# Kernel optimization log

Measured on AMD Instinct MI355X. Metric: run time of the kernel, lower is better.

## Reference

```python
import jax, jax.numpy as jnp
import numpy as np
from jax import lax

B0, C0, H0, W0 = 4, 128, 48, 48
GR = 32  # growth rate
NL = 4   # dense layers


def conv1x1(x, w, b):
    # w: [O, Cin], x: [B, Cin, H, W]
    return jnp.einsum('oc,bchw->bohw', w, x) + b[None, :, None, None]


def conv3x3(x, w, b):
    y = lax.conv_general_dilated(x, w, (1, 1), [(1, 1), (1, 1)],
                                 dimension_numbers=('NCHW', 'OIHW', 'NCHW'))
    return y + b[None, :, None, None]


def batchnorm(x, g, b, eps=1e-5):
    # training-mode BatchNorm2d: batch statistics over (B, H, W)
    mu = jnp.mean(x, axis=(0, 2, 3), keepdims=True)
    var = jnp.var(x, axis=(0, 2, 3), keepdims=True)
    return (x - mu) * lax.rsqrt(var + eps) * g[None, :, None, None] + b[None, :, None, None]


def apply_rope(x):
    B, C, H, W = x.shape
    half = C // 2
    theta = 1.0 / (10000.0 ** (jnp.arange(half, dtype=x.dtype) / half))
    # pos_emb[h, w, j] = (h + w) * theta[j]
    pos = (jnp.arange(H, dtype=x.dtype)[:, None, None]
           + jnp.arange(W, dtype=x.dtype)[None, :, None]) * theta
    cos = jnp.cos(pos).transpose(2, 0, 1)  # [half, H, W]
    sin = jnp.sin(pos).transpose(2, 0, 1)
    xr = x.reshape(B, half, 2, H, W)
    x_re, x_im = xr[:, :, 0], xr[:, :, 1]
    rr = x_re * cos - x_im * sin
    ri = x_re * sin + x_im * cos
    return jnp.stack([rr, ri], axis=2).reshape(B, C, H, W)


def setup_inputs() -> dict:
    key = jax.random.key(0)
    ks = iter(jax.random.split(key, 64))
    def nrm(shape, s=0.05):
        return jax.random.normal(next(ks), shape, jnp.float32) * s
    C = C0
    dc = C + NL * GR  # 256 dense-block output channels
    hid = 4 * C
    d = {
        'x': jax.random.normal(next(ks), (B0, C0, H0, W0), jnp.float32),
        'r_w': nrm((C, C)), 'r_b': jnp.zeros((C,), jnp.float32),
        'k_w': nrm((C, C)), 'k_b': jnp.zeros((C,), jnp.float32),
        'v_w': nrm((C, C)), 'v_b': jnp.zeros((C,), jnp.float32),
        'wc1_w': nrm((C // 4, C, 3, 3)), 'wc1_b': jnp.zeros((C // 4,), jnp.float32),
        'wc2_w': nrm((C, C // 4)), 'wc2_b': jnp.zeros((C,), jnp.float32),
        'u': nrm((C,), 0.1),
        'sn1_w': nrm((dc // 4, dc)), 'sn1_b': jnp.zeros((dc // 4,), jnp.float32),
        'sn2_w': nrm((dc, dc // 4)), 'sn2_b': jnp.zeros((dc,), jnp.float32),
        'lb_w': nrm((C // 4, dc)), 'lb_b': jnp.zeros((C // 4,), jnp.float32),
        'ld_w': nrm((C // 4, dc)), 'ld_b': jnp.zeros((C // 4,), jnp.float32),
        'ps_w': nrm((C, C // 4)), 'ps_b': jnp.zeros((C,), jnp.float32),
        'pq_w': nrm((C, C)), 'pq_b': jnp.zeros((C,), jnp.float32),
        'fc1_w': nrm((hid, C)), 'fc1_b': jnp.zeros((hid,), jnp.float32),
        'fc2_w': nrm((C, hid)), 'fc2_b': jnp.zeros((C,), jnp.float32),
    }
    for i in range(NL):
        cin = C + i * GR
        d[f'db_g{i}'] = jnp.ones((cin,), jnp.float32)
        d[f'db_b{i}'] = jnp.zeros((cin,), jnp.float32)
        d[f'db_w{i}'] = nrm((GR, cin, 3, 3))
        d[f'db_cb{i}'] = jnp.zeros((GR,), jnp.float32)
    return d


def _forward(x, r_w, r_b, k_w, k_b, v_w, v_b, wc1_w, wc1_b, wc2_w, wc2_b, u,
             db_g0, db_b0, db_w0, db_cb0, db_g1, db_b1, db_w1, db_cb1,
             db_g2, db_b2, db_w2, db_cb2, db_g3, db_b3, db_w3, db_cb3,
             sn1_w, sn1_b, sn2_w, sn2_b, lb_w, lb_b, ld_w, ld_b,
             ps_w, ps_b, pq_w, pq_b, fc1_w, fc1_b, fc2_w, fc2_b):
    B, C, H, W = x.shape
    N = H * W
    # decay gate w (hidden is None so it multiplies zeros, kept for fidelity)
    w_gate = jax.nn.sigmoid(conv1x1(jax.nn.relu(conv3x3(x, wc1_w, wc1_b)), wc2_w, wc2_b)).reshape(B, C, N)
    x_rope = apply_rope(x)
    r = jax.nn.sigmoid(conv1x1(x, r_w, r_b))
    k = conv1x1(x_rope, k_w, k_b).reshape(B, C, N)
    v = conv1x1(x_rope, v_w, v_b).reshape(B, C, N)
    zeros = jnp.zeros_like(k)
    new_num = zeros * jnp.exp(-w_gate) + k * v
    new_den = zeros * jnp.exp(-w_gate) + k
    eu = jnp.exp(u)[None, :, None]
    wkv = ((new_num + eu * k * v) / (new_den + eu * k)).reshape(B, C, H, W)
    recursive_output = r * wkv
    # dense block (concat-growth)
    feats = x
    for g, bb, wt, cb in ((db_g0, db_b0, db_w0, db_cb0), (db_g1, db_b1, db_w1, db_cb1),
                          (db_g2, db_b2, db_w2, db_cb2), (db_g3, db_b3, db_w3, db_cb3)):
        h = jax.nn.relu(batchnorm(feats, g, bb))
        feats = jnp.concatenate([feats, conv3x3(h, wt, cb)], axis=1)
    df = feats  # [B, C+4*GR, H, W]
    # adaptive spiking neuron
    tau = jnp.mean(jax.nn.sigmoid(conv1x1(jax.nn.relu(conv1x1(df, sn1_w, sn1_b)), sn2_w, sn2_b)),
                   axis=(2, 3), keepdims=True)
    spike_prob = jax.nn.sigmoid((df - 1.0) * 5.0)
    sf = spike_prob * (df * jnp.exp(-1.0 / (tau + 1e-6))) + (1.0 - spike_prob) * df
    # first attention over N tokens, channels = C//4
    Bf = conv1x1(sf, lb_w, lb_b).reshape(B, -1, N)
    Df = conv1x1(sf, ld_w, ld_b).reshape(B, -1, N)
    attn = jax.nn.softmax(jnp.einsum('bcn,bcm->bnm', Bf, Bf), axis=-1)
    att1 = jnp.einsum('bnm,bcm->bcn', attn, Df).reshape(B, -1, H, W)
    spike_output = conv1x1(att1, ps_w, ps_b)
    combined = recursive_output + spike_output
    # second attention (k/v convs are shared with WKV path)
    Q = conv1x1(combined, pq_w, pq_b).reshape(B, C, N)
    K = conv1x1(combined, k_w, k_b).reshape(B, C, N)
    V = conv1x1(combined, v_w, v_b).reshape(B, C, N)
    scores = jnp.einsum('bcn,bcm->bnm', Q, K) / jnp.sqrt(jnp.asarray(C, x.dtype))
    aw = jax.nn.softmax(scores, axis=-1)
    att2 = jnp.einsum('bnm,bcm->bcn', aw, V).reshape(B, C, H, W)
    x1 = x + att2
    out = x1 + conv1x1(jax.nn.relu(conv1x1(x1, fc1_w, fc1_b)) ** 2, fc2_w, fc2_b)
    return out, new_num, new_den


def reference(x, r_w, r_b, k_w, k_b, v_w, v_b, wc1_w, wc1_b, wc2_w, wc2_b, u,
              db_g0, db_b0, db_w0, db_cb0, db_g1, db_b1, db_w1, db_cb1,
              db_g2, db_b2, db_w2, db_cb2, db_g3, db_b3, db_w3, db_cb3,
              sn1_w, sn1_b, sn2_w, sn2_b, lb_w, lb_b, ld_w, ld_b,
              ps_w, ps_b, pq_w, pq_b, fc1_w, fc1_b, fc2_w, fc2_b):
    return _forward(x, r_w, r_b, k_w, k_b, v_w, v_b, wc1_w, wc1_b, wc2_w, wc2_b, u,
                    db_g0, db_b0, db_w0, db_cb0, db_g1, db_b1, db_w1, db_cb1,
                    db_g2, db_b2, db_w2, db_cb2, db_g3, db_b3, db_w3, db_cb3,
                    sn1_w, sn1_b, sn2_w, sn2_b, lb_w, lb_b, ld_w, ld_b,
                    ps_w, ps_b, pq_w, pq_b, fc1_w, fc1_b, fc2_w, fc2_b)
```

## Files before the change

### kernel.cpp

```cpp
#include <hip/hip_runtime.h>
#include <math.h>

#define BB 4
#define CC 128
#define HH 48
#define WW 48
#define NSP (HH*WW)
#define DCC 256
#define BCN (BB*CC*NSP)
#define KS 6

typedef float f32x4 __attribute__((ext_vector_type(4)));
typedef __bf16 bf16x8 __attribute__((ext_vector_type(8)));
typedef __bf16 bf16x4 __attribute__((ext_vector_type(4)));

__device__ __forceinline__ float sigmf(float v) { return 1.0f / (1.0f + __expf(-v)); }

struct Prep {
  const float* wsrc[13];
  int wlen[13];
  int woff[13];
  const float* psrc[4];
  int pcin[4];
  int poff[4];
  const float* x;
  float* sums;
  float* sums2;
  __bf16* x_t;
  __bf16* xrope_t;
};
__global__ __launch_bounds__(256) void prep_kernel(Prep a, __bf16* __restrict__ wdst,
                                                   __bf16* __restrict__ pdst) {
  __shared__ float lds[32][33];
  __shared__ float rs[4], rs2[4];
  int g = blockIdx.y;
  int idx = blockIdx.x * 256 + threadIdx.x;
  if (g < 13) {
    if (idx < a.wlen[g]) wdst[a.woff[g] + idx] = (__bf16)a.wsrc[g][idx];
  } else if (g < 17) {
    int L = g - 13;
    int cin = a.pcin[L];
    if (idx < 9 * 32 * cin) {
      int c = idx % cin;
      int o = (idx / cin) % 32;
      int tap = idx / (cin * 32);
      pdst[a.poff[L] + idx] = (__bf16)a.psrc[L][((size_t)o * cin + c) * 9 + tap];
    }
  } else if (g == 17) {
    int c = blockIdx.x;
    if (c >= 128) return;
    float s = 0.f, s2 = 0.f;
    for (int i = threadIdx.x; i < BB * NSP; i += 256) {
      int b = i / NSP, n = i % NSP;
      float v = a.x[((size_t)b * 128 + c) * NSP + n];
      s += v;
      s2 += v * v;
    }
#pragma unroll
    for (int off = 32; off > 0; off >>= 1) {
      s += __shfl_down(s, off);
      s2 += __shfl_down(s2, off);
    }
    int wid = threadIdx.x >> 6;
    if ((threadIdx.x & 63) == 0) { rs[wid] = s; rs2[wid] = s2; }
    __syncthreads();
    if (threadIdx.x == 0) {
      a.sums[c] = rs[0] + rs[1] + rs[2] + rs[3];
      a.sums2[c] = rs2[0] + rs2[1] + rs2[2] + rs2[3];
    }
  } else {
    int T = (g - 18) * 256 + blockIdx.x;
    if (T >= 1152) return;
    int b = T / 288;
    int r = T % 288;
    int c0 = (r / 72) * 32;
    int n0 = (r % 72) * 32;
    int tid = threadIdx.x;
    int nn = tid & 31, cs = tid >> 5;
#pragma unroll
    for (int j = 0; j < 4; ++j) {
      int cc = c0 + cs * 4 + j;
      lds[cs * 4 + j][nn] = a.x[((size_t)b * 128 + cc) * NSP + n0 + nn];
    }
    __syncthreads();
    int c = tid & 31, ns = tid >> 5;
#pragma unroll
    for (int j = 0; j < 4; ++j) {
      int n2 = ns * 4 + j;
      float pv = lds[c][n2];
      a.x_t[((size_t)b * NSP + n0 + n2) * 128 + c0 + c] = (__bf16)pv;
      int gc = c0 + c;
      int i = gc >> 1;
      float re = lds[c & ~1][n2];
      float im = lds[c | 1][n2];
      int n = n0 + n2;
      int h = n / WW, w = n % WW;
      float theta = __expf(-9.2103403719761836f * ((float)i) / 64.0f);
      float pos = (float)(h + w) * theta;
      float cs_ = cosf(pos), sn_ = sinf(pos);
      float vr_ = (gc & 1) ? (re * sn_ + im * cs_) : (re * cs_ - im * sn_);
      a.xrope_t[((size_t)b * NSP + n0 + n2) * 128 + c0 + c] = (__bf16)vr_;
    }
  }
}

__global__ __launch_bounds__(256) void kvr_kernel(
    const __bf16* __restrict__ xrope_t, const __bf16* __restrict__ x_t,
    const __bf16* __restrict__ wk, const __bf16* __restrict__ wvp,
    const __bf16* __restrict__ wr,
    const float* __restrict__ k_b, const float* __restrict__ v_b,
    const float* __restrict__ r_b, const float* __restrict__ u,
    float* __restrict__ kden, float* __restrict__ knum, float* __restrict__ rec) {
  int tid = threadIdx.x;
  int wv = tid >> 6, lane = tid & 63;
  int m15 = lane & 15, quad = lane >> 4;
  int b = blockIdx.y;
  int n0 = blockIdx.x * 16;
  int o0 = wv * 32;
  int n = n0 + m15;
  const __bf16* brr = xrope_t + ((size_t)b * NSP + n) * 128 + quad * 8;
  const __bf16* brx = x_t + ((size_t)b * NSP + n) * 128 + quad * 8;
  const __bf16* ak0 = wk + (size_t)(o0 + m15) * 128 + quad * 8;
  const __bf16* ak1 = wk + (size_t)(o0 + 16 + m15) * 128 + quad * 8;
  const __bf16* av0 = wvp + (size_t)(o0 + m15) * 128 + quad * 8;
  const __bf16* av1 = wvp + (size_t)(o0 + 16 + m15) * 128 + quad * 8;
  const __bf16* ar0 = wr + (size_t)(o0 + m15) * 128 + quad * 8;
  const __bf16* ar1 = wr + (size_t)(o0 + 16 + m15) * 128 + quad * 8;
  f32x4 fk[2], fv[2], fr[2];
#pragma unroll
  for (int t = 0; t < 2; ++t) {
    fk[t] = (f32x4){0.f, 0.f, 0.f, 0.f};
    fv[t] = (f32x4){0.f, 0.f, 0.f, 0.f};
    fr[t] = (f32x4){0.f, 0.f, 0.f, 0.f};
  }
#pragma unroll
  for (int kc = 0; kc < 128; kc += 32) {
    bf16x8 br_ = *(const bf16x8*)(brr + kc);
    bf16x8 bx_ = *(const bf16x8*)(brx + kc);
    fk[0] = __builtin_amdgcn_mfma_f32_16x16x32_bf16(*(const bf16x8*)(ak0 + kc), br_, fk[0], 0, 0, 0);
    fk[1] = __builtin_amdgcn_mfma_f32_16x16x32_bf16(*(const bf16x8*)(ak1 + kc), br_, fk[1], 0, 0, 0);
    fv[0] = __builtin_amdgcn_mfma_f32_16x16x32_bf16(*(const bf16x8*)(av0 + kc), br_, fv[0], 0, 0, 0);
    fv[1] = __builtin_amdgcn_mfma_f32_16x16x32_bf16(*(const bf16x8*)(av1 + kc), br_, fv[1], 0, 0, 0);
    fr[0] = __builtin_amdgcn_mfma_f32_16x16x32_bf16(*(const bf16x8*)(ar0 + kc), bx_, fr[0], 0, 0, 0);
    fr[1] = __builtin_amdgcn_mfma_f32_16x16x32_bf16(*(const bf16x8*)(ar1 + kc), bx_, fr[1], 0, 0, 0);
  }
#pragma unroll
  for (int t = 0; t < 2; ++t) {
#pragma unroll
    for (int reg = 0; reg < 4; ++reg) {
      int ol = o0 + t * 16 + quad * 4 + reg;
      float kk = fk[t][reg] + k_b[ol];
      float vv = fv[t][reg] + v_b[ol];
      float rr = sigmf(fr[t][reg] + r_b[ol]);
      float eu = __expf(u[ol]);
      size_t idx = ((size_t)b * 128 + ol) * NSP + n;
      float nv = kk * vv, tt = eu * kk;
      kden[idx] = kk;
      knum[idx] = nv;
      rec[idx] = rr * ((nv + tt * vv) / (kk + tt));
    }
  }
}

template <int OUT>
__device__ __forceinline__ void gemm_store(void* outp, int b, int n, int Oseg,
                                           int obase, int quad, const float* vr) {
  if (OUT == 0) {
    float* op = (float*)outp;
#pragma unroll
    for (int reg = 0; reg < 4; ++reg)
      op[((size_t)b * Oseg + obase + quad * 4 + reg) * NSP + n] = vr[reg];
  } else if (OUT == 1) {
    __bf16* op = (__bf16*)outp;
    bf16x4 pk;
#pragma unroll
    for (int reg = 0; reg < 4; ++reg) pk[reg] = (__bf16)vr[reg];
    *(bf16x4*)(op + ((size_t)b * NSP + n) * Oseg + obase + quad * 4) = pk;
  } else {
    __bf16* op = (__bf16*)outp;
#pragma unroll
    for (int reg = 0; reg < 4; ++reg)
      op[((size_t)b * Oseg + obase + quad * 4 + reg) * NSP + n] = (__bf16)vr[reg];
  }
}

template <int K, int ACT, int OUT0, int OUT1, int OUT2, int SPLITB>
__global__ __launch_bounds__(256) void gemm_mfma_kernel(
    const __bf16* __restrict__ in_t, const __bf16* __restrict__ in_t2,
    const __bf16* __restrict__ wb,
    const float* __restrict__ bias0, const float* __restrict__ bias1,
    const float* __restrict__ bias2,
    const float* __restrict__ add0, const float* __restrict__ add1,
    void* __restrict__ out0, void* __restrict__ out1, void* __restrict__ out2,
    int osplit, int osplit2, int Ototal, float sc0, float sc1, float sc2) {
  int tid = threadIdx.x;
  int wv = tid >> 6, lane = tid & 63;
  int m15 = lane & 15, quad = lane >> 4;
  int b = blockIdx.y;
  int n0 = blockIdx.x * 16;
  int wpb = blockDim.x >> 6;
  int o0 = (blockIdx.z * wpb + wv) * 32;
  if (o0 >= Ototal) return;
  int n = n0 + m15;
  const __bf16* brow = in_t + ((size_t)b * NSP + n) * (SPLITB ? 128 : K) + quad * 8;
  const __bf16* brow2 = SPLITB ? (in_t2 + ((size_t)b * NSP + n) * 128 + quad * 8) : nullptr;
  const __bf16* a0p = wb + (size_t)(o0 + m15) * K + quad * 8;
  const __bf16* a1p = wb + (size_t)(o0 + 16 + m15) * K + quad * 8;
  f32x4 of0 = (f32x4){0.f, 0.f, 0.f, 0.f};
  f32x4 of1 = (f32x4){0.f, 0.f, 0.f, 0.f};
#pragma unroll
  for (int kc = 0; kc < K; kc += 32) {
    bf16x8 bfr;
    if constexpr (SPLITB) {
      bfr = (kc < 128) ? *(const bf16x8*)(brow + kc) : *(const bf16x8*)(brow2 + (kc - 128));
    } else {
      bfr = *(const bf16x8*)(brow + kc);
    }
    bf16x8 a0 = *(const bf16x8*)(a0p + kc);
    bf16x8 a1 = *(const bf16x8*)(a1p + kc);
    of0 = __builtin_amdgcn_mfma_f32_16x16x32_bf16(a0, bfr, of0, 0, 0, 0);
    of1 = __builtin_amdgcn_mfma_f32_16x16x32_bf16(a1, bfr, of1, 0, 0, 0);
  }
  int seg = (o0 >= osplit2) ? 2 : (o0 >= osplit) ? 1 : 0;
  int segb = (seg == 2) ? osplit2 : (seg == 1) ? osplit : 0;
  int sege = (seg == 2) ? Ototal : (seg == 1) ? osplit2 : osplit;
  int Oseg = sege - segb;
  int ol0 = o0 - segb;
  const float* bias = (seg == 2) ? bias2 : (seg == 1) ? bias1 : bias0;
  const float* add = (seg == 2) ? nullptr : (seg == 1) ? add1 : add0;
  void* outp = (seg == 2) ? out2 : (seg == 1) ? out1 : out0;
  float sc = (seg == 2) ? sc2 : (seg == 1) ? sc1 : sc0;
#pragma unroll
  for (int t = 0; t < 2; ++t) {
    f32x4 acc = t ? of1 : of0;
    float vr[4];
#pragma unroll
    for (int reg = 0; reg < 4; ++reg) {
      int ol = ol0 + t * 16 + quad * 4 + reg;
      float v = acc[reg] + bias[ol];
      if (ACT == 1) v = fmaxf(v, 0.0f);
      else if (ACT == 2) v = sigmf(v);
      else if (ACT == 3) { v = fmaxf(v, 0.0f); v = v * v; }
      v *= sc;
      if (add) v += add[((size_t)b * Oseg + ol) * NSP + n];
      vr[reg] = v;
    }
    if constexpr (OUT0 == 3) {
#pragma unroll
      for (int reg = 0; reg < 4; ++reg) {
        float sv = vr[reg];
        sv += __shfl_xor(sv, 1);
        sv += __shfl_xor(sv, 2);
        sv += __shfl_xor(sv, 4);
        sv += __shfl_xor(sv, 8);
        if (m15 == 0)
          ((float*)out0)[((size_t)(b * DCC + ol0 + t * 16 + quad * 4 + reg)) * 144 +
                         blockIdx.x] = sv;
      }
    } else {
      if (seg == 0) gemm_store<OUT0>(outp, b, n, Oseg, ol0 + t * 16, quad, vr);
      else if (seg == 1) gemm_store<OUT1>(outp, b, n, Oseg, ol0 + t * 16, quad, vr);
      else gemm_store<OUT2>(outp, b, n, Oseg, ol0 + t * 16, quad, vr);
    }
  }
}

__global__ __launch_bounds__(128) void lbld_sf_kernel(
    const __bf16* __restrict__ x_t, const __bf16* __restrict__ dense_t,
    const float* __restrict__ taupart, const __bf16* __restrict__ wlb,
    const float* __restrict__ lb_b, const float* __restrict__ ld_b,
    __bf16* __restrict__ Bft, __bf16* __restrict__ Dfb) {
  __shared__ float ef[256];
  int tid = threadIdx.x;
  int b = blockIdx.y;
  for (int ch = tid; ch < 256; ch += 128) {
    const f32x4* tp = (const f32x4*)(taupart + ((size_t)(b * DCC + ch)) * 144);
    f32x4 s4 = (f32x4){0.f, 0.f, 0.f, 0.f};
#pragma unroll
    for (int j = 0; j < 36; ++j) s4 += tp[j];
    float tv = (s4.x + s4.y + s4.z + s4.w) * (1.0f / (float)NSP);
    ef[ch] = __expf(-1.0f / (tv + 1e-6f)) - 1.0f;
  }
  __syncthreads();
  int wv = tid >> 6, lane = tid & 63;
  int m15 = lane & 15, quad = lane >> 4;
  int n0 = blockIdx.x * 16;
  int o0 = wv * 32;
  int n = n0 + m15;
  const __bf16* bx = x_t + ((size_t)b * NSP + n) * 128 + quad * 8;
  const __bf16* bd = dense_t + ((size_t)b * NSP + n) * 128 + quad * 8;
  const __bf16* a0p = wlb + (size_t)(o0 + m15) * 256 + quad * 8;
  const __bf16* a1p = wlb + (size_t)(o0 + 16 + m15) * 256 + quad * 8;
  f32x4 of0 = (f32x4){0.f, 0.f, 0.f, 0.f};
  f32x4 of1 = (f32x4){0.f, 0.f, 0.f, 0.f};
#pragma unroll
  for (int kc = 0; kc < 256; kc += 32) {
    bf16x8 raw = (kc < 128) ? *(const bf16x8*)(bx + kc) : *(const bf16x8*)(bd + (kc - 128));
    bf16x8 sfv;
#pragma unroll
    for (int j = 0; j < 8; ++j) {
      float df = (float)raw[j];
      float sp = sigmf((df - 1.0f) * 5.0f);
      sfv[j] = (__bf16)(df * (1.0f + sp * ef[kc + quad * 8 + j]));
    }
    bf16x8 a0 = *(const bf16x8*)(a0p + kc);
    bf16x8 a1 = *(const bf16x8*)(a1p + kc);
    of0 = __builtin_amdgcn_mfma_f32_16x16x32_bf16(a0, sfv, of0, 0, 0, 0);
    of1 = __builtin_amdgcn_mfma_f32_16x16x32_bf16(a1, sfv, of1, 0, 0, 0);
  }
  if (o0 == 0) {
#pragma unroll
    for (int t = 0; t < 2; ++t) {
      f32x4 acc = t ? of1 : of0;
      bf16x4 pk;
#pragma unroll
      for (int reg = 0; reg < 4; ++reg) pk[reg] = (__bf16)(acc[reg] + lb_b[t * 16 + quad * 4 + reg]);
      *(bf16x4*)(Bft + ((size_t)b * NSP + n) * 32 + t * 16 + quad * 4) = pk;
    }
  } else {
#pragma unroll
    for (int t = 0; t < 2; ++t) {
      f32x4 acc = t ? of1 : of0;
#pragma unroll
      for (int reg = 0; reg < 4; ++reg) {
        int ol = t * 16 + quad * 4 + reg;
        Dfb[((size_t)b * 32 + ol) * NSP + n] = (__bf16)(acc[reg] + ld_b[ol]);
      }
    }
  }
}

__global__ __launch_bounds__(256) void bnrelu_t_kernel(
    const float* __restrict__ src, size_t bstride, int gcoff,
    const float* __restrict__ sums, const float* __restrict__ sums2,
    const float* __restrict__ cpart,
    const float* __restrict__ g, const float* __restrict__ bb,
    __bf16* __restrict__ ht) {
  __shared__ float lds[32][33];
  __shared__ float fst[64];
  int b = blockIdx.z;
  int n0 = blockIdx.x * 32;
  int c0 = blockIdx.y * 32;
  int tid = threadIdx.x;

  if (cpart) {
    __shared__ float tmp[4][64];
    int r = tid & 63, sl = tid >> 6;
    const float* cp = cpart + (size_t)r * 576 + sl * 144;
    float a = 0.f;
#pragma unroll 4
    for (int j = 0; j < 144; ++j) a += cp[j];
    tmp[sl][r] = a;
    __syncthreads();
    if (tid < 64) fst[tid] = tmp[0][tid] + tmp[1][tid] + tmp[2][tid] + tmp[3][tid];
    __syncthreads();
  }

  int nn = tid & 31, cs = tid >> 5;
#pragma unroll
  for (int j = 0; j < 4; ++j) {
    int cc = c0 + cs * 4 + j;
    lds[cs * 4 + j][nn] = src[(size_t)b * bstride + (size_t)cc * NSP + n0 + nn];
  }
  __syncthreads();
  int c = tid & 31, ns = tid >> 5;
  int gc = gcoff + c0 + c;
  const float inv = 1.0f / (float)(BB * NSP);
  float S = cpart ? fst[c] : sums[gc];
  float S2 = cpart ? fst[32 + c] : sums2[gc];
  float m = S * inv;
  float var = S2 * inv - m * m;
  float sc_ = rsqrtf(var + 1e-5f) * g[gc];
  float sh_ = bb[gc] - m * sc_;
#pragma unroll
  for (int j = 0; j < 4; ++j) {
    int n2 = ns * 4 + j;
    float v = fmaxf(lds[c][n2] * sc_ + sh_, 0.0f);
    ht[((size_t)b * NSP + n0 + n2) * DCC + gc] = (__bf16)v;
  }
}

template <int Cin>
__global__ __launch_bounds__(256) void conv3x3_mfma_kernel(
    const __bf16* __restrict__ ht, const __bf16* __restrict__ wb,
    const float* __restrict__ cb, float* __restrict__ feats, int cout0,
    __bf16* __restrict__ dense_t, float* __restrict__ cpart) {
  constexpr int KCin = Cin / 32;
  __shared__ float red[4][64][8];
  int tid = threadIdx.x;
  int wv = tid >> 6, lane = tid & 63;
  int m15 = lane & 15, quad = lane >> 4;
  int b = blockIdx.y;
  int n0 = blockIdx.x * 16;
  int n = n0 + m15;
  int h = n / WW, w = n % WW;
  f32x4 of0 = (f32x4){0.f, 0.f, 0.f, 0.f};
  f32x4 of1 = (f32x4){0.f, 0.f, 0.f, 0.f};
  const __bf16* htb = ht + (size_t)b * NSP * DCC;
  const bf16x8 zf = {};
  for (int ci = wv; ci < 9 * KCin; ci += 4) {
    int tap = ci / KCin;
    int kc = (ci % KCin) * 32;
    int dh = tap / 3 - 1, dw = tap % 3 - 1;
    bool valid = ((unsigned)(h + dh) < HH) && ((unsigned)(w + dw) < WW);
    int pa = valid ? (n + dh * WW + dw) : 0;
    bf16x8 bfr = *(const bf16x8*)(htb + (size_t)pa * DCC + kc + quad * 8);
    if (!valid) bfr = zf;
    const __bf16* wt = wb + (size_t)tap * 32 * Cin + kc + quad * 8;
    bf16x8 a0 = *(const bf16x8*)(wt + (size_t)m15 * Cin);
    bf16x8 a1 = *(const bf16x8*)(wt + (size_t)(16 + m15) * Cin);
    of0 = __builtin_amdgcn_mfma_f32_16x16x32_bf16(a0, bfr, of0, 0, 0, 0);
    of1 = __builtin_amdgcn_mfma_f32_16x16x32_bf16(a1, bfr, of1, 0, 0, 0);
  }
  float* myred = red[wv][lane];
#pragma unroll
  for (int reg = 0; reg < 4; ++reg) {
    myred[reg] = of0[reg];
    myred[4 + reg] = of1[reg];
  }
  __syncthreads();
  if (wv == 0) {
    int dloc = cout0 - 128;
    __bf16* dt = dense_t + ((size_t)b * NSP + n) * 128 + dloc;
#pragma unroll
    for (int reg = 0; reg < 4; ++reg) {
      int o = quad * 4 + reg;
      float v0 = red[0][lane][reg] + red[1][lane][reg] + red[2][lane][reg] +
                 red[3][lane][reg] + cb[o];
      float v1 = red[0][lane][4 + reg] + red[1][lane][4 + reg] + red[2][lane][4 + reg] +
                 red[3][lane][4 + reg] + cb[16 + o];
      feats[((size_t)b * DCC + cout0 + o) * NSP + n] = v0;
      feats[((size_t)b * DCC + cout0 + 16 + o) * NSP + n] = v1;
      dt[o] = (__bf16)v0;
      dt[16 + o] = (__bf16)v1;
      if (cpart) {
        float a0 = v0, q0 = v0 * v0, a1 = v1, q1 = v1 * v1;
#pragma unroll
        for (int mk = 1; mk < 16; mk <<= 1) {
          a0 += __shfl_xor(a0, mk);
          q0 += __shfl_xor(q0, mk);
          a1 += __shfl_xor(a1, mk);
          q1 += __shfl_xor(q1, mk);
        }
        if (m15 == 0) {
          int pidx = blockIdx.y * 144 + blockIdx.x;
          cpart[(size_t)o * 576 + pidx] = a0;
          cpart[(size_t)(32 + o) * 576 + pidx] = q0;
          cpart[(size_t)(16 + o) * 576 + pidx] = a1;
          cpart[(size_t)(48 + o) * 576 + pidx] = q1;
        }
      }
    }
  }
}

template <int CD>
__global__ __launch_bounds__(256) void attn_part_kernel(
    const __bf16* __restrict__ Qt, const __bf16* __restrict__ Kt,
    const __bf16* __restrict__ Vb, __bf16* __restrict__ Op,
    float* __restrict__ lp) {
  constexpr int NC = CD / 16;
  constexpr int KC = CD / 32;
  constexpr int KEYS = NSP / KS;
  constexpr int KP = CD + 4;
  constexpr int VP = 36;
  __shared__ __bf16 kl[32][KP];
  __shared__ __bf16 vl[CD][VP];
  __shared__ float pt[4][16][36];
  int tid = threadIdx.x;
  int wv = tid >> 6, lane = tid & 63;
  int m15 = lane & 15, quad = lane >> 4;
  int b = blockIdx.y, ks = blockIdx.z;
  int n0 = blockIdx.x * 64 + wv * 16;

  bf16x8 qf[KC];
  const __bf16* qrow = Qt + ((size_t)b * NSP + n0 + m15) * CD + quad * 8;
#pragma unroll
  for (int kc = 0; kc < KC; ++kc) qf[kc] = *(const bf16x8*)(qrow + kc * 32);

  f32x4 of[NC];
#pragma unroll
  for (int i = 0; i < NC; ++i) of[i] = (f32x4){0.f, 0.f, 0.f, 0.f};
  float l0 = 0.f, l1 = 0.f, l2 = 0.f, l3 = 0.f;

  const __bf16* Kb = Kt + (size_t)b * NSP * CD;
  const __bf16* Vbb = Vb + (size_t)b * CD * NSP;
  float(*ptw)[36] = pt[wv];

  for (int m0 = ks * KEYS; m0 < (ks + 1) * KEYS; m0 += 32) {
    __syncthreads();
    for (int i = tid; i < 32 * CD / 8; i += 256) {
      int row = i / (CD / 8);
      int cc8 = (i % (CD / 8)) * 8;
      *(bf16x8*)&kl[row][cc8] = *(const bf16x8*)(Kb + (size_t)(m0 + row) * CD + cc8);
    }
    for (int i = tid; i < CD * 4; i += 256) {
      int ch = i / 4;
      int k8 = (i % 4) * 8;
      *(bf16x8*)&vl[ch][k8] = *(const bf16x8*)(Vbb + (size_t)ch * NSP + m0 + k8);
    }
    __syncthreads();
    f32x4 s[2];
#pragma unroll
    for (int t = 0; t < 2; ++t) {
      f32x4 acc = (f32x4){0.f, 0.f, 0.f, 0.f};
#pragma unroll
      for (int kc = 0; kc < KC; ++kc) {
        bf16x8 kf = *(const bf16x8*)&kl[t * 16 + m15][kc * 32 + quad * 8];
        acc = __builtin_amdgcn_mfma_f32_16x16x32_bf16(qf[kc], kf, acc, 0, 0, 0);
      }
      s[t] = acc;
    }
#pragma unroll
    for (int t = 0; t < 2; ++t) {
      float e0 = __expf(s[t].x), e1 = __expf(s[t].y), e2 = __expf(s[t].z), e3 = __expf(s[t].w);
      l0 += e0; l1 += e1; l2 += e2; l3 += e3;
      ptw[quad * 4 + 0][t * 16 + m15] = e0;
      ptw[quad * 4 + 1][t * 16 + m15] = e1;
      ptw[quad * 4 + 2][t * 16 + m15] = e2;
      ptw[quad * 4 + 3][t * 16 + m15] = e3;
    }
    const float* prow = &ptw[m15][quad * 8];
    f32x4 pa = *(const f32x4*)(prow);
    f32x4 pb = *(const f32x4*)(prow + 4);
    bf16x8 pf;
    pf[0] = (__bf16)pa.x; pf[1] = (__bf16)pa.y; pf[2] = (__bf16)pa.z; pf[3] = (__bf16)pa.w;
    pf[4] = (__bf16)pb.x; pf[5] = (__bf16)pb.y; pf[6] = (__bf16)pb.z; pf[7] = (__bf16)pb.w;
#pragma unroll
    for (int ct = 0; ct < NC; ++ct) {
      bf16x8 vf = *(const bf16x8*)&vl[ct * 16 + m15][quad * 8];
      of[ct] = __builtin_amdgcn_mfma_f32_16x16x32_bf16(pf, vf, of[ct], 0, 0, 0);
    }
  }

#pragma unroll
  for (int off = 1; off < 16; off <<= 1) {
    l0 += __shfl_xor(l0, off);
    l1 += __shfl_xor(l1, off);
    l2 += __shfl_xor(l2, off);
    l3 += __shfl_xor(l3, off);
  }
  float* lpb = lp + (size_t)(ks * BB + b) * NSP + n0;
  if (m15 == 0) {
    lpb[quad * 4 + 0] = l0;
    lpb[quad * 4 + 1] = l1;
    lpb[quad * 4 + 2] = l2;
    lpb[quad * 4 + 3] = l3;
  }
  __bf16* Ob = Op + (size_t)(ks * BB + b) * CD * NSP;
#pragma unroll
  for (int ct = 0; ct < NC; ++ct) {
    bf16x4 pk;
#pragma unroll
    for (int reg = 0; reg < 4; ++reg) pk[reg] = (__bf16)of[ct][reg];
    *(bf16x4*)(Ob + (size_t)(ct * 16 + m15) * NSP + n0 + quad * 4) = pk;
  }
}

__global__ __launch_bounds__(256) void combine32_kernel(const __bf16* __restrict__ Op,
                                                        const float* __restrict__ lp,
                                                        __bf16* __restrict__ att1_t) {
  __shared__ float lds[32][33];
  int b = blockIdx.z;
  int n0 = blockIdx.x * 32;
  int tid = threadIdx.x;
  int nn = tid & 31, cs = tid >> 5;
  float ltot = 0.f;
#pragma unroll
  for (int ks = 0; ks < KS; ++ks) ltot += lp[(size_t)(ks * BB + b) * NSP + n0 + nn];
  float linv = 1.0f / ltot;
#pragma unroll
  for (int j = 0; j < 4; ++j) {
    int cc = cs * 4 + j;
    float s = 0.f;
#pragma unroll
    for (int ks = 0; ks < KS; ++ks)
      s += (float)Op[((size_t)(ks * BB + b) * 32 + cc) * NSP + n0 + nn];
    lds[cc][nn] = s * linv;
  }
  __syncthreads();
  int c = tid & 31, ns = tid >> 5;
#pragma unroll
  for (int j = 0; j < 4; ++j) {
    int n2 = ns * 4 + j;
    att1_t[((size_t)b * NSP + n0 + n2) * 32 + c] = (__bf16)lds[c][n2];
  }
}

__global__ __launch_bounds__(256) void combine128_kernel(
    const __bf16* __restrict__ Op, const float* __restrict__ lp,
    const float* __restrict__ x, float* __restrict__ x1, __bf16* __restrict__ x1_t) {
  __shared__ float lds[32][33];
  int b = blockIdx.z;
  int n0 = blockIdx.x * 32;
  int c0 = blockIdx.y * 32;
  int tid = threadIdx.x;
  int nn = tid & 31, cs = tid >> 5;
  float ltot = 0.f;
#pragma unroll
  for (int ks = 0; ks < KS; ++ks) ltot += lp[(size_t)(ks * BB + b) * NSP + n0 + nn];
  float linv = 1.0f / ltot;
#pragma unroll
  for (int j = 0; j < 4; ++j) {
    int gc = c0 + cs * 4 + j;
    float s = 0.f;
#pragma unroll
    for (int ks = 0; ks < KS; ++ks)
      s += (float)Op[((size_t)(ks * BB + b) * CC + gc) * NSP + n0 + nn];
    float v = s * linv + x[((size_t)b * CC + gc) * NSP + n0 + nn];
    lds[cs * 4 + j][nn] = v;
    x1[((size_t)b * CC + gc) * NSP + n0 + nn] = v;
  }
  __syncthreads();
  int c = tid & 31, ns = tid >> 5;
#pragma unroll
  for (int j = 0; j < 4; ++j) {
    int n2 = ns * 4 + j;
    x1_t[((size_t)b * NSP + n0 + n2) * CC + c0 + c] = (__bf16)lds[c][n2];
  }
}

extern "C" void kernel_launch(void* const* d_in, const int* in_sizes, int n_in,
                              void* d_out, int out_size, void* d_ws, size_t ws_size,
                              hipStream_t stream) {
  const float* x = (const float*)d_in[0];
  const float* r_w = (const float*)d_in[1];
  const float* r_b = (const float*)d_in[2];
  const float* k_w = (const float*)d_in[3];
  const float* k_b = (const float*)d_in[4];
  const float* v_w = (const float*)d_in[5];
  const float* v_b = (const float*)d_in[6];
  const float* u = (const float*)d_in[11];
  const float* sn1_w = (const float*)d_in[12];
  const float* sn1_b = (const float*)d_in[13];
  const float* sn2_w = (const float*)d_in[14];
  const float* sn2_b = (const float*)d_in[15];
  const float* lb_w = (const float*)d_in[16];
  const float* lb_b = (const float*)d_in[17];
  const float* ld_w = (const float*)d_in[18];
  const float* ld_b = (const float*)d_in[19];
  const float* ps_w = (const float*)d_in[20];
  const float* ps_b = (const float*)d_in[21];
  const float* pq_w = (const float*)d_in[22];
  const float* pq_b = (const float*)d_in[23];
  const float* fc1_w = (const float*)d_in[24];
  const float* fc1_b = (const float*)d_in[25];
  const float* fc2_w = (const float*)d_in[26];
  const float* fc2_b = (const float*)d_in[27];
  const float* db_g[4] = {(const float*)d_in[28], (const float*)d_in[32],
                          (const float*)d_in[36], (const float*)d_in[40]};
  const float* db_b[4] = {(const float*)d_in[29], (const float*)d_in[33],
                          (const float*)d_in[37], (const float*)d_in[41]};
  const float* db_w[4] = {(const float*)d_in[30], (const float*)d_in[34],
                          (const float*)d_in[38], (const float*)d_in[42]};
  const float* db_cb[4] = {(const float*)d_in[31], (const float*)d_in[35],
                           (const float*)d_in[39], (const float*)d_in[43]};

  float* outp = (float*)d_out;
  float* knum = outp + BCN;
  float* kden = outp + 2 * (size_t)BCN;

  float* ws = (float*)d_ws;
  const size_t F_FEATS = 0;
  const size_t F_REC = 4718592;
  const size_t F_V = 5898240;
  const size_t F_R = 7077888;
  const size_t F_XR = 8257536;
  const size_t F_XT = 8847360;
  const size_t F_DFB = 9437184;
  const size_t F_AT1T = 9584640;
  const size_t F_CT = 9732096;
  const size_t F_LP = 10321920;
  const size_t F_WB = 10434048;
  const size_t F_WB3 = 10575360;
  const size_t F_STATS = 10676736;
  const size_t F_CPART = 10677248;
  const size_t F_TAUP = 10714112;
  float* sums = ws + F_STATS;
  float* sums2 = ws + F_STATS + 256;
  float* cpart = ws + F_CPART;
  float* taupart = ws + F_TAUP;
  float* lp = ws + F_LP;
  __bf16* wbase = (__bf16*)(ws + F_WB);
  __bf16* wb3 = (__bf16*)(ws + F_WB3);
  const int W_KV = 0;
  const int W_R = 32768;
  const int W_SN1 = 49152;
  const int W_SN2 = 65536;
  const int W_LBLD = 81920;
  const int W_PS = 98304;
  const int W_PQK = 102400;
  const int W_FC1 = 151552;
  const int W_FC2 = 217088;
  const int W3_OFF[4] = {0, 36864, 82944, 138240};

  dim3 blk(256);
  __bf16* xrope_t = (__bf16*)(ws + F_XR);
  __bf16* x_t = (__bf16*)(ws + F_XT);

  Prep pp;
  pp.wsrc[0] = k_w;    pp.wlen[0] = 16384; pp.woff[0] = W_KV;
  pp.wsrc[1] = v_w;    pp.wlen[1] = 16384; pp.woff[1] = W_KV + 16384;
  pp.wsrc[2] = r_w;    pp.wlen[2] = 16384; pp.woff[2] = W_R;
  pp.wsrc[3] = sn1_w;  pp.wlen[3] = 16384; pp.woff[3] = W_SN1;
  pp.wsrc[4] = sn2_w;  pp.wlen[4] = 16384; pp.woff[4] = W_SN2;
  pp.wsrc[5] = lb_w;   pp.wlen[5] = 8192;  pp.woff[5] = W_LBLD;
  pp.wsrc[6] = ld_w;   pp.wlen[6] = 8192;  pp.woff[6] = W_LBLD + 8192;
  pp.wsrc[7] = ps_w;   pp.wlen[7] = 4096;  pp.woff[7] = W_PS;
  pp.wsrc[8] = pq_w;   pp.wlen[8] = 16384; pp.woff[8] = W_PQK;
  pp.wsrc[9] = k_w;    pp.wlen[9] = 16384; pp.woff[9] = W_PQK + 16384;
  pp.wsrc[10] = v_w;   pp.wlen[10] = 16384; pp.woff[10] = W_PQK + 32768;
  pp.wsrc[11] = fc1_w; pp.wlen[11] = 65536; pp.woff[11] = W_FC1;
  pp.wsrc[12] = fc2_w; pp.wlen[12] = 65536; pp.woff[12] = W_FC2;
  for (int i = 0; i < 4; ++i) {
    pp.psrc[i] = db_w[i];
    pp.pcin[i] = 128 + 32 * i;
    pp.poff[i] = W3_OFF[i];
  }
  pp.x = x;
  pp.sums = sums;
  pp.sums2 = sums2;
  pp.x_t = x_t;
  pp.xrope_t = xrope_t;
  prep_kernel<<<dim3(256, 23), blk, 0, stream>>>(pp, wbase, wb3);

  kvr_kernel<<<dim3(144, 4), blk, 0, stream>>>(
      xrope_t, x_t, wbase + W_KV, wbase + W_KV + 16384, wbase + W_R,
      k_b, v_b, r_b, u, kden, knum, ws + F_REC);

  __bf16* ht = (__bf16*)(ws + F_V);
  __bf16* dense_t = (__bf16*)(ws + F_R);
  bnrelu_t_kernel<<<dim3(72, 4, 4), blk, 0, stream>>>(x, (size_t)128 * NSP, 0, sums, sums2,
                                                      nullptr, db_g[0], db_b[0], ht);
  conv3x3_mfma_kernel<128><<<dim3(144, 4), blk, 0, stream>>>(
      ht, wb3 + W3_OFF[0], db_cb[0], ws + F_FEATS, 128, dense_t, cpart);
  for (int i = 1; i < 4; ++i) {
    int cin = 128 + 32 * i;
    bnrelu_t_kernel<<<dim3(72, 1, 4), blk, 0, stream>>>(
        ws + F_FEATS + (size_t)(cin - 32) * NSP, (size_t)256 * NSP, cin - 32,
        nullptr, nullptr, cpart, db_g[i], db_b[i], ht);
    float* cp = (i < 3) ? cpart : nullptr;
    switch (cin) {
      case 160: conv3x3_mfma_kernel<160><<<dim3(144, 4), blk, 0, stream>>>(ht, wb3 + W3_OFF[i], db_cb[i], ws + F_FEATS, cin, dense_t, cp); break;
      case 192: conv3x3_mfma_kernel<192><<<dim3(144, 4), blk, 0, stream>>>(ht, wb3 + W3_OFF[i], db_cb[i], ws + F_FEATS, cin, dense_t, cp); break;
      default:  conv3x3_mfma_kernel<224><<<dim3(144, 4), blk, 0, stream>>>(ht, wb3 + W3_OFF[i], db_cb[i], ws + F_FEATS, cin, dense_t, cp); break;
    }
  }

  __bf16* z1_t = (__bf16*)(ws + F_XR);
  gemm_mfma_kernel<256, 1, 1, 1, 0, 1><<<dim3(144, 4, 1), dim3(128), 0, stream>>>(
      x_t, dense_t, wbase + W_SN1, sn1_b, sn1_b, nullptr, nullptr, nullptr,
      z1_t, z1_t, nullptr, 64, 64, 64, 1.f, 1.f, 1.f);
  gemm_mfma_kernel<64, 2, 3, 3, 0, 0><<<dim3(144, 4, 2), blk, 0, stream>>>(
      z1_t, nullptr, wbase + W_SN2, sn2_b, sn2_b, nullptr, nullptr, nullptr,
      taupart, taupart, nullptr, 256, 256, 256, 1.f, 1.f, 1.f);
  __bf16* Bft = (__bf16*)(ws + F_XT);
  Bft = (__bf16*)(ws + F_CT + 294912);
  __bf16* Dfb = (__bf16*)(ws + F_DFB);
  lbld_sf_kernel<<<dim3(144, 4), dim3(128), 0, stream>>>(
      x_t, dense_t, taupart, wbase + W_LBLD, lb_b, ld_b, Bft, Dfb);
  __bf16* Opart = (__bf16*)(ws + F_FEATS);
  attn_part_kernel<32><<<dim3(36, 4, KS), blk, 0, stream>>>(Bft, Bft, Dfb, Opart, lp);
  __bf16* att1_t = (__bf16*)(ws + F_AT1T);
  combine32_kernel<<<dim3(72, 1, 4), blk, 0, stream>>>(Opart, lp, att1_t);
  __bf16* comb_t = (__bf16*)(ws + F_CT);
  gemm_mfma_kernel<32, 0, 1, 1, 0, 0><<<dim3(144, 4, 1), blk, 0, stream>>>(
      att1_t, nullptr, wbase + W_PS, ps_b, ps_b, nullptr, ws + F_REC, ws + F_REC,
      comb_t, comb_t, nullptr, 128, 128, 128, 1.f, 1.f, 1.f);

  __bf16* Qt = (__bf16*)(ws + F_XR);
  __bf16* K2t = (__bf16*)(ws + F_XT);
  __bf16* V2b = (__bf16*)(ws + F_V);
  gemm_mfma_kernel<128, 0, 1, 1, 2, 0><<<dim3(144, 4, 3), blk, 0, stream>>>(
      comb_t, nullptr, wbase + W_PQK, pq_b, k_b, v_b, nullptr, nullptr,
      Qt, K2t, V2b, 128, 256, 384, 0.08838834764831845f, 1.f, 1.f);
  attn_part_kernel<128><<<dim3(36, 4, KS), blk, 0, stream>>>(Qt, K2t, V2b, Opart, lp);
  float* x1 = ws + F_R;
  __bf16* x1_t = (__bf16*)(ws + F_CT);
  combine128_kernel<<<dim3(72, 4, 4), blk, 0, stream>>>(Opart, lp, x, x1, x1_t);

  __bf16* h_t = (__bf16*)(ws + F_FEATS);
  gemm_mfma_kernel<128, 3, 1, 1, 0, 0><<<dim3(144, 4, 4), blk, 0, stream>>>(
      x1_t, nullptr, wbase + W_FC1, fc1_b, fc1_b, nullptr, nullptr, nullptr,
      h_t, h_t, nullptr, 512, 512, 512, 1.f, 1.f, 1.f);
  gemm_mfma_kernel<512, 0, 0, 0, 0, 0><<<dim3(144, 4, 1), blk, 0, stream>>>(
      h_t, nullptr, wbase + W_FC2, fc2_b, fc2_b, nullptr, x1, x1,
      outp, outp, nullptr, 128, 128, 128, 1.f, 1.f, 1.f);
}
```

Before: 412.7 us.

## Fuse BatchNorm+ReLU into conv3x3 operand loads and drop fp32 feature writes

Removes the separate bnrelu transpose kernels and applies the batch-norm scale/shift and ReLU on the fly while loading conv3x3 input fragments from x_t and dense_t. Each layer's per-channel statistics are finalized inside the next conv kernel, and the fp32 feature map writes are dropped in favour of vectorized bf16 dense_t stores. Also lowers the attention key split from 6 to 4. The cost is redundant BN arithmetic per MFMA tile and a changed split of iterations across waves.

```diff
diff --git a/kernel.cpp b/kernel.cpp
--- a/kernel.cpp
+++ b/kernel.cpp
@@ -8,7 +8,7 @@
 #define NSP (HH*WW)
 #define DCC 256
 #define BCN (BB*CC*NSP)
-#define KS 6
+#define KS 4
 
 typedef float f32x4 __attribute__((ext_vector_type(4)));
 typedef __bf16 bf16x8 __attribute__((ext_vector_type(8)));
@@ -330,64 +330,55 @@
   }
 }
 
-__global__ __launch_bounds__(256) void bnrelu_t_kernel(
-    const float* __restrict__ src, size_t bstride, int gcoff,
-    const float* __restrict__ sums, const float* __restrict__ sums2,
-    const float* __restrict__ cpart,
-    const float* __restrict__ g, const float* __restrict__ bb,
-    __bf16* __restrict__ ht) {
-  __shared__ float lds[32][33];
-  __shared__ float fst[64];
-  int b = blockIdx.z;
-  int n0 = blockIdx.x * 32;
-  int c0 = blockIdx.y * 32;
+template <int Cin>
+__global__ __launch_bounds__(256) void convbn_kernel(
+    const __bf16* __restrict__ x_t, const __bf16* __restrict__ dense_t,
+    const __bf16* __restrict__ wb, const float* __restrict__ cb,
+    float* __restrict__ sums, float* __restrict__ sums2,
+    const float* __restrict__ cpart_in,
+    const float* __restrict__ g, const float* __restrict__ bbp,
+    __bf16* __restrict__ dense_out, float* __restrict__ cpart_out, int cout0) {
+  constexpr int KCin = Cin / 32;
+  constexpr int NIT = 9 * KCin;
+  __shared__ float red[4][64][8];
+  __shared__ float scsh[2][Cin];
+  __shared__ float tred[64][4];
+  __shared__ float fin[64];
   int tid = threadIdx.x;
-
-  if (cpart) {
-    __shared__ float tmp[4][64];
-    int r = tid & 63, sl = tid >> 6;
-    const float* cp = cpart + (size_t)r * 576 + sl * 144;
-    float a = 0.f;
-#pragma unroll 4
-    for (int j = 0; j < 144; ++j) a += cp[j];
-    tmp[sl][r] = a;
+  const float inv = 1.0f / (float)(BB * NSP);
+
+  if (cpart_in) {
+    int row = tid >> 2, sl = tid & 3;
+    const f32x4* cp = (const f32x4*)(cpart_in + (size_t)row * 576 + sl * 144);
+    f32x4 s4 = (f32x4){0.f, 0.f, 0.f, 0.f};
+#pragma unroll
+    for (int j = 0; j < 36; ++j) s4 += cp[j];
+    tred[row][sl] = s4.x + s4.y + s4.z + s4.w;
     __syncthreads();
-    if (tid < 64) fst[tid] = tmp[0][tid] + tmp[1][tid] + tmp[2][tid] + tmp[3][tid];
+    if (tid < 64) fin[tid] = tred[tid][0] + tred[tid][1] + tred[tid][2] + tred[tid][3];
     __syncthreads();
-  }
-
-  int nn = tid & 31, cs = tid >> 5;
-#pragma unroll
-  for (int j = 0; j < 4; ++j) {
-    int cc = c0 + cs * 4 + j;
-    lds[cs * 4 + j][nn] = src[(size_t)b * bstride + (size_t)cc * NSP + n0 + nn];
+    if (blockIdx.x == 0 && blockIdx.y == 0 && tid < 32) {
+      sums[Cin - 32 + tid] = fin[tid];
+      sums2[Cin - 32 + tid] = fin[32 + tid];
+    }
+  }
+  for (int ch = tid; ch < Cin; ch += 256) {
+    float S, S2;
+    if (cpart_in && ch >= Cin - 32) {
+      S = fin[ch - (Cin - 32)];
+      S2 = fin[ch - (Cin - 32) + 32];
+    } else {
+      S = sums[ch];
+      S2 = sums2[ch];
+    }
+    float m = S * inv;
+    float var = S2 * inv - m * m;
+    float sc_ = rsqrtf(var + 1e-5f) * g[ch];
+    scsh[0][ch] = sc_;
+    scsh[1][ch] = bbp[ch] - m * sc_;
   }
   __syncthreads();
-  int c = tid & 31, ns = tid >> 5;
-  int gc = gcoff + c0 + c;
-  const float inv = 1.0f / (float)(BB * NSP);
-  float S = cpart ? fst[c] : sums[gc];
-  float S2 = cpart ? fst[32 + c] : sums2[gc];
-  float m = S * inv;
-  float var = S2 * inv - m * m;
-  float sc_ = rsqrtf(var + 1e-5f) * g[gc];
-  float sh_ = bb[gc] - m * sc_;
-#pragma unroll
-  for (int j = 0; j < 4; ++j) {
-    int n2 = ns * 4 + j;
-    float v = fmaxf(lds[c][n2] * sc_ + sh_, 0.0f);
-    ht[((size_t)b * NSP + n0 + n2) * DCC + gc] = (__bf16)v;
-  }
-}
-
-template <int Cin>
-__global__ __launch_bounds__(256) void conv3x3_mfma_kernel(
-    const __bf16* __restrict__ ht, const __bf16* __restrict__ wb,
-    const float* __restrict__ cb, float* __restrict__ feats, int cout0,
-    __bf16* __restrict__ dense_t, float* __restrict__ cpart) {
-  constexpr int KCin = Cin / 32;
-  __shared__ float red[4][64][8];
-  int tid = threadIdx.x;
+
   int wv = tid >> 6, lane = tid & 63;
   int m15 = lane & 15, quad = lane >> 4;
   int b = blockIdx.y;
@@ -396,15 +387,37 @@
   int h = n / WW, w = n % WW;
   f32x4 of0 = (f32x4){0.f, 0.f, 0.f, 0.f};
   f32x4 of1 = (f32x4){0.f, 0.f, 0.f, 0.f};
-  const __bf16* htb = ht + (size_t)b * NSP * DCC;
+  const __bf16* bx_ = x_t + (size_t)b * NSP * 128;
+  const __bf16* bd_ = dense_t + (size_t)b * NSP * 128;
   const bf16x8 zf = {};
-  for (int ci = wv; ci < 9 * KCin; ci += 4) {
-    int tap = ci / KCin;
-    int kc = (ci % KCin) * 32;
+  int begin = (wv * NIT) / 4, end = ((wv + 1) * NIT) / 4;
+  int cur = -1;
+  float bsc[8], bsh[8];
+  const __bf16* base = nullptr;
+  for (int ci = begin; ci < end; ++ci) {
+    int chunk = ci / 9;
+    int tap = ci - chunk * 9;
+    int kc = chunk * 32;
+    if (chunk != cur) {
+      cur = chunk;
+      int cc = kc + quad * 8;
+#pragma unroll
+      for (int j = 0; j < 8; ++j) {
+        bsc[j] = scsh[0][cc + j];
+        bsh[j] = scsh[1][cc + j];
+      }
+      base = (cc < 128) ? (bx_ + cc) : (bd_ + cc - 128);
+    }
     int dh = tap / 3 - 1, dw = tap % 3 - 1;
     bool valid = ((unsigned)(h + dh) < HH) && ((unsigned)(w + dw) < WW);
     int pa = valid ? (n + dh * WW + dw) : 0;
-    bf16x8 bfr = *(const bf16x8*)(htb + (size_t)pa * DCC + kc + quad * 8);
+    bf16x8 raw = *(const bf16x8*)(base + (size_t)pa * 128);
+    bf16x8 bfr;
+#pragma unroll
+    for (int j = 0; j < 8; ++j) {
+      float v = fmaxf((float)raw[j] * bsc[j] + bsh[j], 0.0f);
+      bfr[j] = (__bf16)v;
+    }
     if (!valid) bfr = zf;
     const __bf16* wt = wb + (size_t)tap * 32 * Cin + kc + quad * 8;
     bf16x8 a0 = *(const bf16x8*)(wt + (size_t)m15 * Cin);
@@ -421,7 +434,9 @@
   __syncthreads();
   if (wv == 0) {
     int dloc = cout0 - 128;
-    __bf16* dt = dense_t + ((size_t)b * NSP + n) * 128 + dloc;
+    __bf16* dt = dense_out + ((size_t)b * NSP + n) * 128 + dloc;
+    bf16x4 pk0, pk1;
+    float sv[4][4];
 #pragma unroll
     for (int reg = 0; reg < 4; ++reg) {
       int o = quad * 4 + reg;
@@ -429,12 +444,19 @@
                  red[3][lane][reg] + cb[o];
       float v1 = red[0][lane][4 + reg] + red[1][lane][4 + reg] + red[2][lane][4 + reg] +
                  red[3][lane][4 + reg] + cb[16 + o];
-      feats[((size_t)b * DCC + cout0 + o) * NSP + n] = v0;
-      feats[((size_t)b * DCC + cout0 + 16 + o) * NSP + n] = v1;
-      dt[o] = (__bf16)v0;
-      dt[16 + o] = (__bf16)v1;
-      if (cpart) {
-        float a0 = v0, q0 = v0 * v0, a1 = v1, q1 = v1 * v1;
+      pk0[reg] = (__bf16)v0;
+      pk1[reg] = (__bf16)v1;
+      sv[reg][0] = v0;
+      sv[reg][1] = v0 * v0;
+      sv[reg][2] = v1;
+      sv[reg][3] = v1 * v1;
+    }
+    *(bf16x4*)(dt + quad * 4) = pk0;
+    *(bf16x4*)(dt + 16 + quad * 4) = pk1;
+    if (cpart_out) {
+#pragma unroll
+      for (int reg = 0; reg < 4; ++reg) {
+        float a0 = sv[reg][0], q0 = sv[reg][1], a1 = sv[reg][2], q1 = sv[reg][3];
 #pragma unroll
         for (int mk = 1; mk < 16; mk <<= 1) {
           a0 += __shfl_xor(a0, mk);
@@ -443,11 +465,12 @@
           q1 += __shfl_xor(q1, mk);
         }
         if (m15 == 0) {
+          int o = quad * 4 + reg;
           int pidx = blockIdx.y * 144 + blockIdx.x;
-          cpart[(size_t)o * 576 + pidx] = a0;
-          cpart[(size_t)(32 + o) * 576 + pidx] = q0;
-          cpart[(size_t)(16 + o) * 576 + pidx] = a1;
-          cpart[(size_t)(48 + o) * 576 + pidx] = q1;
+          cpart_out[(size_t)o * 576 + pidx] = a0;
+          cpart_out[(size_t)(32 + o) * 576 + pidx] = q0;
+          cpart_out[(size_t)(16 + o) * 576 + pidx] = a1;
+          cpart_out[(size_t)(48 + o) * 576 + pidx] = q1;
         }
       }
     }
@@ -674,11 +697,12 @@
   const size_t F_WB = 10434048;
   const size_t F_WB3 = 10575360;
   const size_t F_STATS = 10676736;
-  const size_t F_CPART = 10677248;
   const size_t F_TAUP = 10714112;
   float* sums = ws + F_STATS;
   float* sums2 = ws + F_STATS + 256;
-  float* cpart = ws + F_CPART;
+  float* cpart0 = ws + F_FEATS;
+  float* cpart1 = cpart0 + 36864;
+  float* cpart2 = cpart1 + 36864;
   float* taupart = ws + F_TAUP;
   float* lp = ws + F_LP;
   __bf16* wbase = (__bf16*)(ws + F_WB);
@@ -728,24 +752,19 @@
       xrope_t, x_t, wbase + W_KV, wbase + W_KV + 16384, wbase + W_R,
       k_b, v_b, r_b, u, kden, knum, ws + F_REC);
 
-  __bf16* ht = (__bf16*)(ws + F_V);
   __bf16* dense_t = (__bf16*)(ws + F_R);
-  bnrelu_t_kernel<<<dim3(72, 4, 4), blk, 0, stream>>>(x, (size_t)128 * NSP, 0, sums, sums2,
-                                                      nullptr, db_g[0], db_b[0], ht);
-  conv3x3_mfma_kernel<128><<<dim3(144, 4), blk, 0, stream>>>(
-      ht, wb3 + W3_OFF[0], db_cb[0], ws + F_FEATS, 128, dense_t, cpart);
-  for (int i = 1; i < 4; ++i) {
-    int cin = 128 + 32 * i;
-    bnrelu_t_kernel<<<dim3(72, 1, 4), blk, 0, stream>>>(
-        ws + F_FEATS + (size_t)(cin - 32) * NSP, (size_t)256 * NSP, cin - 32,
-        nullptr, nullptr, cpart, db_g[i], db_b[i], ht);
-    float* cp = (i < 3) ? cpart : nullptr;
-    switch (cin) {
-      case 160: conv3x3_mfma_kernel<160><<<dim3(144, 4), blk, 0, stream>>>(ht, wb3 + W3_OFF[i], db_cb[i], ws + F_FEATS, cin, dense_t, cp); break;
-      case 192: conv3x3_mfma_kernel<192><<<dim3(144, 4), blk, 0, stream>>>(ht, wb3 + W3_OFF[i], db_cb[i], ws + F_FEATS, cin, dense_t, cp); break;
-      default:  conv3x3_mfma_kernel<224><<<dim3(144, 4), blk, 0, stream>>>(ht, wb3 + W3_OFF[i], db_cb[i], ws + F_FEATS, cin, dense_t, cp); break;
-    }
-  }
+  convbn_kernel<128><<<dim3(144, 4), blk, 0, stream>>>(
+      x_t, dense_t, wb3 + W3_OFF[0], db_cb[0], sums, sums2, nullptr,
+      db_g[0], db_b[0], dense_t, cpart0, 128);
+  convbn_kernel<160><<<dim3(144, 4), blk, 0, stream>>>(
+      x_t, dense_t, wb3 + W3_OFF[1], db_cb[1], sums, sums2, cpart0,
+      db_g[1], db_b[1], dense_t, cpart1, 160);
+  convbn_kernel<192><<<dim3(144, 4), blk, 0, stream>>>(
+      x_t, dense_t, wb3 + W3_OFF[2], db_cb[2], sums, sums2, cpart1,
+      db_g[2], db_b[2], dense_t, cpart2, 192);
+  convbn_kernel<224><<<dim3(144, 4), blk, 0, stream>>>(
+      x_t, dense_t, wb3 + W3_OFF[3], db_cb[3], sums, sums2, cpart2,
+      db_g[3], db_b[3], dense_t, nullptr, 224);
 
   __bf16* z1_t = (__bf16*)(ws + F_XR);
   gemm_mfma_kernel<256, 1, 1, 1, 0, 1><<<dim3(144, 4, 1), dim3(128), 0, stream>>>(
@@ -754,8 +773,7 @@
   gemm_mfma_kernel<64, 2, 3, 3, 0, 0><<<dim3(144, 4, 2), blk, 0, stream>>>(
       z1_t, nullptr, wbase + W_SN2, sn2_b, sn2_b, nullptr, nullptr, nullptr,
       taupart, taupart, nullptr, 256, 256, 256, 1.f, 1.f, 1.f);
-  __bf16* Bft = (__bf16*)(ws + F_XT);
-  Bft = (__bf16*)(ws + F_CT + 294912);
+  __bf16* Bft = (__bf16*)(ws + F_CT + 294912);
   __bf16* Dfb = (__bf16*)(ws + F_DFB);
   lbld_sf_kernel<<<dim3(144, 4), dim3(128), 0, stream>>>(
       x_t, dense_t, taupart, wbase + W_LBLD, lb_b, ld_b, Bft, Dfb);
```

Measured after the change: 413.6 us. No clear change (+0.2%).
